# Kernel tuning notes

Measured on AMD Instinct MI355X. Metric: run time of the kernel, lower is better.

The kernel has to match this reference:

```python
import jax, jax.numpy as jnp
import numpy as np

V, E, H, B, T = 50257, 1024, 1024, 64, 512  # vocab, embed, hidden, batch, steps
PADDING_TOKEN = 0


def setup_inputs() -> dict:
    key = jax.random.key(0)
    ks = jax.random.split(key, 6)
    s = 0.02
    emb = jax.random.normal(ks[0], (V, E), jnp.float32) * s
    emb = emb.at[PADDING_TOKEN].set(0.0)  # padding_idx row is zero
    W_ih = jax.random.normal(ks[1], (4 * H, E), jnp.float32) * s   # torch LSTMCell weight_ih
    W_hh = jax.random.normal(ks[2], (4 * H, H), jnp.float32) * s   # torch LSTMCell weight_hh
    W_cls = jax.random.normal(ks[3], (V, H), jnp.float32) * s      # classifier weight [out,in]
    b_cls = jnp.zeros((V,), jnp.float32)                            # classifier bias
    batch_reviews = jax.random.randint(ks[4], (B, T), 0, V)
    return dict(batch_reviews=batch_reviews, emb=emb, W_ih=W_ih, W_hh=W_hh,
                W_cls=W_cls, b_cls=b_cls)


def _lstm_scan(x_tbe, W_ih, W_hh):
    # torch.nn.LSTMCell math (bias=False); gate order: i, f, g, o
    Bn = x_tbe.shape[1]
    Hn = W_hh.shape[1]

    def cell(carry, x_be):
        h, c = carry
        gates = x_be @ W_ih.T + h @ W_hh.T              # [B, 4H]
        i, f, g, o = jnp.split(gates, 4, axis=-1)
        c2 = jax.nn.sigmoid(f) * c + jax.nn.sigmoid(i) * jnp.tanh(g)
        h2 = jax.nn.sigmoid(o) * jnp.tanh(c2)
        return (h2, c2), None

    init = (jnp.zeros((Bn, Hn), x_tbe.dtype), jnp.zeros((Bn, Hn), x_tbe.dtype))
    (h, c), _ = jax.lax.scan(cell, init, x_tbe)
    return h, c


def reference(batch_reviews, emb, W_ih, W_hh, W_cls, b_cls):
    x = emb[batch_reviews]               # [B, T, E] embedding lookup
    x_tbe = jnp.transpose(x, (1, 0, 2))  # [T, B, E] for time-major scan
    h, c = _lstm_scan(x_tbe, W_ih, W_hh) # final (h, c) state only
    logits = h @ W_cls.T + b_cls         # [B, V]
    return logits, h, c
```

## Files before the change

### kernel.cpp

```cpp
#include <hip/hip_runtime.h>

#define Bn 64
#define Tn 512
#define En 1024
#define Hn 1024
#define Vn 50257
#define CHUNK 64
#define NCHUNK (Tn / CHUNK)
#define AGENT __HIP_MEMORY_SCOPE_AGENT

typedef __attribute__((ext_vector_type(8))) short short8;
typedef __attribute__((ext_vector_type(4))) float f32x4;
typedef __attribute__((ext_vector_type(4))) unsigned int u32x4;

__device__ __forceinline__ unsigned short f2bf(float f) {
    union { float f; unsigned u; } x; x.f = f;
    unsigned r = x.u + 0x7FFFu + ((x.u >> 16) & 1u);
    return (unsigned short)(r >> 16);
}
__device__ __forceinline__ float bf2f(unsigned short u) {
    union { unsigned u; float f; } x; x.u = ((unsigned)u) << 16; return x.f;
}
__device__ __forceinline__ float sigm(float x) { return 1.0f / (1.0f + __expf(-x)); }
__device__ __forceinline__ float tanh_fast(float x) {
    float e = __expf(2.0f * x);
    return (e - 1.0f) / (e + 1.0f);
}

#define LDH(dst, base, IMM)                                                  \
    asm volatile("global_load_dwordx4 %0, %1, off offset:" #IMM " sc0 sc1"   \
                 : "=v"(dst) : "v"(base) : "memory")
#define VMW(N) do { asm volatile("s_waitcnt vmcnt(" #N ")" ::: "memory");    \
                    __builtin_amdgcn_sched_barrier(0); } while (0)
#define ISSUE_GRP(buf, O0, O1, O2, O3)                                       \
    do {                                                                     \
        LDH((buf)[0], ap0, O0); LDH((buf)[1], ap0, O1);                      \
        LDH((buf)[2], ap0, O2); LDH((buf)[3], ap0, O3);                      \
        LDH((buf)[4], ap1, O0); LDH((buf)[5], ap1, O1);                      \
        LDH((buf)[6], ap1, O2); LDH((buf)[7], ap1, O3);                      \
    } while (0)
#define MFMA_GRP(buf, jb)                                                    \
    do {                                                                     \
        _Pragma("unroll")                                                    \
        for (int jj = 0; jj < 4; ++jj) {                                     \
            union { u32x4 u; short8 s; } f0, f1;                             \
            f0.u = (buf)[jj]; f1.u = (buf)[4 + jj];                          \
            acc[0][0] = __builtin_amdgcn_mfma_f32_16x16x32_bf16(f0.s, breg[0][(jb) + jj], acc[0][0], 0, 0, 0); \
            acc[0][1] = __builtin_amdgcn_mfma_f32_16x16x32_bf16(f0.s, breg[1][(jb) + jj], acc[0][1], 0, 0, 0); \
            acc[1][0] = __builtin_amdgcn_mfma_f32_16x16x32_bf16(f1.s, breg[0][(jb) + jj], acc[1][0], 0, 0, 0); \
            acc[1][1] = __builtin_amdgcn_mfma_f32_16x16x32_bf16(f1.s, breg[1][(jb) + jj], acc[1][1], 0, 0, 0); \
        }                                                                    \
    } while (0)

__global__ __launch_bounds__(256)
void cvt_f32_bf16(const float* __restrict__ src, unsigned short* __restrict__ dst, int n4) {
    int i = blockIdx.x * 256 + threadIdx.x;
    if (i < n4) {
        float4 v = reinterpret_cast<const float4*>(src)[i];
        ushort4 o;
        o.x = f2bf(v.x); o.y = f2bf(v.y); o.z = f2bf(v.z); o.w = f2bf(v.w);
        reinterpret_cast<ushort4*>(dst)[i] = o;
    }
}

__global__ __launch_bounds__(256)
void gather_x(const int* __restrict__ tokens, const float* __restrict__ emb,
              unsigned short* __restrict__ X, int t0) {
    const int r = blockIdx.x;
    const int trel = r >> 6, b = r & 63;
    const int tok = tokens[b * Tn + t0 + trel];
    const float* src = emb + (size_t)tok * En;
    const int k = threadIdx.x * 4;
    float4 v = *reinterpret_cast<const float4*>(src + k);
    ushort4 o;
    o.x = f2bf(v.x); o.y = f2bf(v.y); o.z = f2bf(v.z); o.w = f2bf(v.w);
    *reinterpret_cast<ushort4*>(X + (size_t)r * En + k) = o;
}

__device__ __forceinline__ void gemm_tile(
    const unsigned short* __restrict__ X, const unsigned short* __restrict__ Wih,
    unsigned short* __restrict__ G, int bx, int by,
    unsigned short (*As)[72], unsigned short (*Bs)[72], int tid)
{
    const int w = tid >> 6, l = tid & 63;
    const int wr = w >> 1, wc = w & 1;
    const int koff = (l >> 4) * 8;

    f32x4 acc[4][4];
#pragma unroll
    for (int i = 0; i < 4; ++i)
#pragma unroll
        for (int j = 0; j < 4; ++j) acc[i][j] = (f32x4){0.f, 0.f, 0.f, 0.f};

    for (int kk = 0; kk < En / 64; ++kk) {
        __syncthreads();
#pragma unroll
        for (int j = 0; j < 4; ++j) {
            const int u = tid * 4 + j;
            const int row = u >> 3, ku = (u & 7) * 8;
            *reinterpret_cast<short8*>(&As[row][ku]) =
                *reinterpret_cast<const short8*>(X + (size_t)(by * 128 + row) * En + kk * 64 + ku);
            *reinterpret_cast<short8*>(&Bs[row][ku]) =
                *reinterpret_cast<const short8*>(Wih + (size_t)(bx * 128 + row) * En + kk * 64 + ku);
        }
        __syncthreads();

#pragma unroll
        for (int kc = 0; kc < 2; ++kc) {
            const int k0 = kc * 32 + koff;
            short8 af[4], bf[4];
#pragma unroll
            for (int i = 0; i < 4; ++i)
                af[i] = *reinterpret_cast<const short8*>(&As[wr * 64 + i * 16 + (l & 15)][k0]);
#pragma unroll
            for (int j = 0; j < 4; ++j)
                bf[j] = *reinterpret_cast<const short8*>(&Bs[wc * 64 + j * 16 + (l & 15)][k0]);
#pragma unroll
            for (int i = 0; i < 4; ++i)
#pragma unroll
                for (int j = 0; j < 4; ++j)
                    acc[i][j] = __builtin_amdgcn_mfma_f32_16x16x32_bf16(af[i], bf[j], acc[i][j], 0, 0, 0);
        }
    }

    const int rr = 4 * (l >> 4);
#pragma unroll
    for (int i = 0; i < 4; ++i) {
        const int row = by * 128 + wr * 64 + i * 16 + rr;
#pragma unroll
        for (int j = 0; j < 4; ++j) {
            const int col = bx * 128 + wc * 64 + j * 16 + (l & 15);
#pragma unroll
            for (int r = 0; r < 4; ++r)
                G[(size_t)(row + r) * 4096 + col] = f2bf(acc[i][j][r]);
        }
    }
}

__global__ __launch_bounds__(256)
void gemm_gin(const unsigned short* __restrict__ X, const unsigned short* __restrict__ Wih,
              unsigned short* __restrict__ G) {
    __shared__ __align__(16) unsigned short As[128][72];
    __shared__ __align__(16) unsigned short Bs[128][72];
    gemm_tile(X, Wih, G, blockIdx.x & 31, blockIdx.x >> 5, As, Bs, threadIdx.x);
}

__global__ __launch_bounds__(256, 1)
void lstm_fused(const unsigned short* __restrict__ Gcur, unsigned short* __restrict__ Gnext,
                const unsigned short* __restrict__ Xnext, const unsigned short* __restrict__ Wih,
                const unsigned short* __restrict__ Whh,
                unsigned short* __restrict__ h0, unsigned short* __restrict__ h1,
                float* __restrict__ c_state, unsigned* __restrict__ flags, int t0, int do_gemm,
                float* __restrict__ out_h, float* __restrict__ out_c)
{
    __shared__ __align__(16) char smem[2 * 128 * 72 * 2];

    const int tid = threadIdx.x;

    if (blockIdx.x >= 128) {
        if (!do_gemm) return;
        unsigned short (*As)[72] = reinterpret_cast<unsigned short(*)[72]>(smem);
        unsigned short (*Bs)[72] = reinterpret_cast<unsigned short(*)[72]>(smem + 128 * 72 * 2);
        const int base = (blockIdx.x - 128) * 8;
        for (int tt = 0; tt < 8; ++tt) {
            const int tile = base + tt;
            gemm_tile(Xnext, Wih, Gnext, tile & 31, tile >> 5, As, Bs, tid);
        }
        return;
    }

    typedef float RedT[2][2][64][4];
    RedT* red = reinterpret_cast<RedT*>(smem);

    const int b = blockIdx.x;
    const int w = tid >> 6, l = tid & 63;
    const int kh = w & 1, rh = w >> 1;
    const int koff = (l >> 4) * 8;
    const int lc = l & 15;
    const int hcol = b * 8 + (l & 7);

    short8 breg[2][16];
#pragma unroll
    for (int ct = 0; ct < 2; ++ct) {
        const int gate = ct * 2 + (lc >> 3);
        const unsigned short* wrow = Whh + ((size_t)gate * Hn + (b * 8 + (lc & 7))) * Hn;
#pragma unroll
        for (int j = 0; j < 16; ++j)
            breg[ct][j] = *reinterpret_cast<const short8*>(wrow + (kh * 16 + j) * 32 + koff);
    }

    float c_reg[2][4];
    if (kh == 0) {
#pragma unroll
        for (int rt = 0; rt < 2; ++rt)
#pragma unroll
            for (int r = 0; r < 4; ++r)
                c_reg[rt][r] = c_state[(rh * 32 + rt * 16 + ((l >> 4) << 2) + r) * Hn + hcol];
    }

    const int sg = lc >> 3;
    const int gc0 = sg * Hn + hcol;
    const int gc1 = (2 + sg) * Hn + hcol;

    unsigned short gp0[2][4], gp1[2][4];
    if (kh == 0) {
#pragma unroll
        for (int rt = 0; rt < 2; ++rt) {
            const int rowbase = rh * 32 + rt * 16 + ((l >> 4) << 2);
#pragma unroll
            for (int r = 0; r < 4; ++r) {
                gp0[rt][r] = Gcur[(size_t)(rowbase + r) * 4096 + gc0];
                gp1[rt][r] = Gcur[(size_t)(rowbase + r) * 4096 + gc1];
            }
        }
    }

    const unsigned* myflag = &flags[(kh * 64 + l) * 32];

    for (int s = 0; s < CHUNK; ++s) {
        const int t = t0 + s;
        const unsigned short* hin = (t & 1) ? h1 : h0;
        unsigned short* hout = (t & 1) ? h0 : h1;

        {
            const unsigned target = (unsigned)t;
            int guard = 0;
            while (__hip_atomic_load(myflag, __ATOMIC_RELAXED, AGENT) < target &&
                   guard < (1 << 16)) {
                __builtin_amdgcn_s_sleep(1);
                ++guard;
            }
        }
        __builtin_amdgcn_sched_barrier(0);

        const unsigned short* ap0 =
            hin + (size_t)(rh * 32 + (l & 15)) * Hn + kh * 512 + koff;
        const unsigned short* ap1 =
            hin + (size_t)(rh * 32 + 16 + (l & 15)) * Hn + kh * 512 + koff;

        f32x4 acc[2][2];
        acc[0][0] = acc[0][1] = acc[1][0] = acc[1][1] = (f32x4){0.f, 0.f, 0.f, 0.f};

        u32x4 bufA[8], bufB[8], bufC[8], bufD[8];
        ISSUE_GRP(bufA, 0,   64,  128, 192);
        ISSUE_GRP(bufB, 256, 320, 384, 448);
        ISSUE_GRP(bufC, 512, 576, 640, 704);
        ISSUE_GRP(bufD, 768, 832, 896, 960);

        VMW(24); MFMA_GRP(bufA, 0);
        VMW(16); MFMA_GRP(bufB, 4);
        VMW(8);  MFMA_GRP(bufC, 8);
        VMW(0);  MFMA_GRP(bufD, 12);

        if (kh == 1) {
#pragma unroll
            for (int rt = 0; rt < 2; ++rt)
#pragma unroll
                for (int ct = 0; ct < 2; ++ct)
                    *reinterpret_cast<f32x4*>(&red[rh][rt][ct][l][0]) = acc[rt][ct];
        }
        __syncthreads();

        if (kh == 0) {
#pragma unroll
            for (int rt = 0; rt < 2; ++rt) {
                const int rowbase = rh * 32 + rt * 16 + ((l >> 4) << 2);
                f32x4 a0 = acc[rt][0] + *reinterpret_cast<f32x4*>(&red[rh][rt][0][l][0]);
                f32x4 a1 = acc[rt][1] + *reinterpret_cast<f32x4*>(&red[rh][rt][1][l][0]);
#pragma unroll
                for (int r = 0; r < 4; ++r) {
                    float v0 = a0[r] + bf2f(gp0[rt][r]);
                    float v1 = a1[r] + bf2f(gp1[rt][r]);
                    float p0 = __shfl_xor(v0, 8);
                    float p1 = __shfl_xor(v1, 8);
                    float iv = (l & 8) ? p0 : v0;
                    float fv = (l & 8) ? v0 : p0;
                    float gv = (l & 8) ? p1 : v1;
                    float ov = (l & 8) ? v1 : p1;
                    float cn = sigm(fv) * c_reg[rt][r] + sigm(iv) * tanh_fast(gv);
                    float hn = sigm(ov) * tanh_fast(cn);
                    c_reg[rt][r] = cn;
                    unsigned hb = f2bf(hn);
                    unsigned partner = (unsigned)__shfl_xor((int)hb, 1);
                    if (!(l & 8) && !(l & 1)) {
                        unsigned val = (hb & 0xFFFFu) | (partner << 16);
                        __hip_atomic_store(
                            (unsigned*)(hout + (size_t)(rowbase + r) * Hn + hcol),
                            val, __ATOMIC_RELAXED, AGENT);
                    }
                    if (t == Tn - 1 && !(l & 8)) {
                        out_h[(rowbase + r) * Hn + hcol] = hn;
                        out_c[(rowbase + r) * Hn + hcol] = cn;
                    }
                }
            }
        }

        asm volatile("s_waitcnt vmcnt(0)" ::: "memory");
        __syncthreads();
        if (tid == 0)
            __hip_atomic_store(&flags[b * 32], (unsigned)(t + 1), __ATOMIC_RELAXED, AGENT);

        if (kh == 0 && s + 1 < CHUNK) {
            const unsigned short* Gt = Gcur + (size_t)(s + 1) * Bn * 4096;
#pragma unroll
            for (int rt = 0; rt < 2; ++rt) {
                const int rowbase = rh * 32 + rt * 16 + ((l >> 4) << 2);
#pragma unroll
                for (int r = 0; r < 4; ++r) {
                    gp0[rt][r] = Gt[(size_t)(rowbase + r) * 4096 + gc0];
                    gp1[rt][r] = Gt[(size_t)(rowbase + r) * 4096 + gc1];
                }
            }
        }
    }

    if (kh == 0 && !(l & 8)) {
#pragma unroll
        for (int rt = 0; rt < 2; ++rt)
#pragma unroll
            for (int r = 0; r < 4; ++r)
                c_state[(rh * 32 + rt * 16 + ((l >> 4) << 2) + r) * Hn + hcol] = c_reg[rt][r];
    }
}

__global__ __launch_bounds__(256)
void classifier(const unsigned short* __restrict__ h,
                const float* __restrict__ Wcls, const float* __restrict__ bcls,
                float* __restrict__ logits)
{
    __shared__ __align__(16) unsigned short Al[64][72];
    __shared__ __align__(16) unsigned short Bl[64][72];

    const int tid = threadIdx.x;
    const int v0 = blockIdx.x * 64;
    const int w = tid >> 6, l = tid & 63;
    const int lrow = tid >> 2, q = tid & 3;
    const int v = v0 + lrow;

    const unsigned short* hrow = h + lrow * Hn;
    const float* wrow = Wcls + (size_t)v * Hn;

    f32x4 acc[4];
#pragma unroll
    for (int ct = 0; ct < 4; ++ct) acc[ct] = (f32x4){0.f, 0.f, 0.f, 0.f};

    const int arow = w * 16 + (l & 15);
    const int koff = (l >> 4) * 8;

    for (int ch = 0; ch < 16; ++ch) {
        const int k0 = ch * 64;
        __syncthreads();
#pragma unroll
        for (int i2 = 0; i2 < 4; ++i2) {
            const int k = q * 4 + i2 * 16;
            *reinterpret_cast<ushort4*>(&Al[lrow][k]) =
                *reinterpret_cast<const ushort4*>(hrow + k0 + k);
            if (v < Vn) {
                float4 x = *reinterpret_cast<const float4*>(wrow + k0 + k);
                Bl[lrow][k + 0] = f2bf(x.x); Bl[lrow][k + 1] = f2bf(x.y);
                Bl[lrow][k + 2] = f2bf(x.z); Bl[lrow][k + 3] = f2bf(x.w);
            } else {
                ushort4 z; z.x = z.y = z.z = z.w = 0;
                *reinterpret_cast<ushort4*>(&Bl[lrow][k]) = z;
            }
        }
        __syncthreads();

        short8 a0 = *reinterpret_cast<const short8*>(&Al[arow][koff]);
        short8 a1 = *reinterpret_cast<const short8*>(&Al[arow][32 + koff]);
#pragma unroll
        for (int ct = 0; ct < 4; ++ct) {
            const int bcol = ct * 16 + (l & 15);
            short8 b0 = *reinterpret_cast<const short8*>(&Bl[bcol][koff]);
            short8 b1 = *reinterpret_cast<const short8*>(&Bl[bcol][32 + koff]);
            acc[ct] = __builtin_amdgcn_mfma_f32_16x16x32_bf16(a0, b0, acc[ct], 0, 0, 0);
            acc[ct] = __builtin_amdgcn_mfma_f32_16x16x32_bf16(a1, b1, acc[ct], 0, 0, 0);
        }
    }

    const int rr0 = w * 16 + (l >> 4) * 4;
#pragma unroll
    for (int ct = 0; ct < 4; ++ct) {
        const int vv = v0 + ct * 16 + (l & 15);
        if (vv < Vn) {
            float bb = bcls[vv];
#pragma unroll
            for (int r = 0; r < 4; ++r)
                logits[(size_t)(rr0 + r) * Vn + vv] = acc[ct][r] + bb;
        }
    }
}

extern "C" void kernel_launch(void* const* d_in, const int* in_sizes, int n_in,
                              void* d_out, int out_size, void* d_ws, size_t ws_size,
                              hipStream_t stream)
{
    const int*   tokens = (const int*)d_in[0];
    const float* emb    = (const float*)d_in[1];
    const float* W_ih   = (const float*)d_in[2];
    const float* W_hh   = (const float*)d_in[3];
    const float* W_cls  = (const float*)d_in[4];
    const float* b_cls  = (const float*)d_in[5];
    float* out = (float*)d_out;

    char* ws = (char*)d_ws;
    unsigned short* hbuf0 = (unsigned short*)ws;
    unsigned short* hbuf1 = (unsigned short*)(ws + 131072);
    float*          cst   = (float*)(ws + 262144);
    unsigned*       flags = (unsigned*)(ws + 524288);
    unsigned short* Wih_b = (unsigned short*)(ws + 540672);
    unsigned short* Whh_b = (unsigned short*)(ws + 540672 + 8388608);
    unsigned short* Xb    = (unsigned short*)(ws + 540672 + 2 * 8388608);
    unsigned short* Gb0   = (unsigned short*)(ws + 540672 + 3 * 8388608);
    unsigned short* Gb1   = (unsigned short*)(ws + 540672 + 3 * 8388608 + 33554432);

    hipMemsetAsync(ws, 0, 540672, stream);

    const int n4 = (4 * Hn * En) / 4;
    cvt_f32_bf16<<<n4 / 256, 256, 0, stream>>>(W_ih, Wih_b, n4);
    cvt_f32_bf16<<<n4 / 256, 256, 0, stream>>>(W_hh, Whh_b, n4);

    float* out_h = out + (size_t)Bn * Vn;
    float* out_c = out_h + Bn * Hn;

    gather_x<<<CHUNK * Bn, 256, 0, stream>>>(tokens, emb, Xb, 0);
    gemm_gin<<<32 * 32, 256, 0, stream>>>(Xb, Wih_b, Gb0);

    unsigned short* Gbuf[2] = {Gb0, Gb1};
    for (int c = 0; c < NCHUNK; ++c) {
        const int do_gemm = (c + 1 < NCHUNK) ? 1 : 0;
        if (do_gemm)
            gather_x<<<CHUNK * Bn, 256, 0, stream>>>(tokens, emb, Xb, (c + 1) * CHUNK);
        lstm_fused<<<256, 256, 0, stream>>>(Gbuf[c & 1], Gbuf[(c + 1) & 1], Xb,
                                            Wih_b, Whh_b, hbuf0, hbuf1,
                                            cst, flags, c * CHUNK, do_gemm,
                                            out_h, out_c);
    }

    classifier<<<(Vn + 63) / 64, 256, 0, stream>>>(hbuf0, W_cls, b_cls, out);
}
```

Measured before the change: 4.258 ms.

## Split recurrent matvec into front/back K-halves with partial-sum handoff and step-major gate layout

The 128 recurrent blocks are reorganised: each of 64 front blocks owns 16 hidden columns (all four gates) and the first K half, while 64 back blocks compute the second K half and publish fp32 partials through global memory under a separate flag. Only front blocks do the cell update and signal the h-ready flags, so each step waits on 64 flags instead of 128, polled with a wave-wide any. The input-gate GEMM now writes a time/column-major layout, so per-step gate preloads become vector loads. The extra partial-sum handoff adds a global round trip and a second dependency chain to every timestep.

```diff
diff --git a/kernel.cpp b/kernel.cpp
--- a/kernel.cpp
+++ b/kernel.cpp
@@ -30,6 +30,9 @@
 #define LDH(dst, base, IMM)                                                  \
     asm volatile("global_load_dwordx4 %0, %1, off offset:" #IMM " sc0 sc1"   \
                  : "=v"(dst) : "v"(base) : "memory")
+#define STHI(addr, data, IMM)                                                \
+    asm volatile("global_store_dwordx4 %0, %1, off offset:" #IMM " sc0 sc1"  \
+                 :: "v"(addr), "v"(data) : "memory")
 #define VMW(N) do { asm volatile("s_waitcnt vmcnt(" #N ")" ::: "memory");    \
                     __builtin_amdgcn_sched_barrier(0); } while (0)
 #define ISSUE_GRP(buf, O0, O1, O2, O3)                                       \
@@ -39,16 +42,17 @@
         LDH((buf)[4], ap1, O0); LDH((buf)[5], ap1, O1);                      \
         LDH((buf)[6], ap1, O2); LDH((buf)[7], ap1, O3);                      \
     } while (0)
-#define MFMA_GRP(buf, jb)                                                    \
+#define MFMA_G4(buf, jb)                                                     \
     do {                                                                     \
         _Pragma("unroll")                                                    \
         for (int jj = 0; jj < 4; ++jj) {                                     \
             union { u32x4 u; short8 s; } f0, f1;                             \
             f0.u = (buf)[jj]; f1.u = (buf)[4 + jj];                          \
-            acc[0][0] = __builtin_amdgcn_mfma_f32_16x16x32_bf16(f0.s, breg[0][(jb) + jj], acc[0][0], 0, 0, 0); \
-            acc[0][1] = __builtin_amdgcn_mfma_f32_16x16x32_bf16(f0.s, breg[1][(jb) + jj], acc[0][1], 0, 0, 0); \
-            acc[1][0] = __builtin_amdgcn_mfma_f32_16x16x32_bf16(f1.s, breg[0][(jb) + jj], acc[1][0], 0, 0, 0); \
-            acc[1][1] = __builtin_amdgcn_mfma_f32_16x16x32_bf16(f1.s, breg[1][(jb) + jj], acc[1][1], 0, 0, 0); \
+            _Pragma("unroll")                                                \
+            for (int ct = 0; ct < 4; ++ct) {                                 \
+                acc[0][ct] = __builtin_amdgcn_mfma_f32_16x16x32_bf16(f0.s, breg[ct][(jb) + jj], acc[0][ct], 0, 0, 0); \
+                acc[1][ct] = __builtin_amdgcn_mfma_f32_16x16x32_bf16(f1.s, breg[ct][(jb) + jj], acc[1][ct], 0, 0, 0); \
+            }                                                                \
         }                                                                    \
     } while (0)
 
@@ -79,7 +83,7 @@
 
 __device__ __forceinline__ void gemm_tile(
     const unsigned short* __restrict__ X, const unsigned short* __restrict__ Wih,
-    unsigned short* __restrict__ G, int bx, int by,
+    unsigned short* __restrict__ G2, int bx, int by,
     unsigned short (*As)[72], unsigned short (*Bs)[72], int tid)
 {
     const int w = tid >> 6, l = tid & 63;
@@ -126,23 +130,25 @@
     const int rr = 4 * (l >> 4);
 #pragma unroll
     for (int i = 0; i < 4; ++i) {
-        const int row = by * 128 + wr * 64 + i * 16 + rr;
+        const int grow = by * 128 + wr * 64 + i * 16 + rr;
+        const int sI = grow >> 6, br = grow & 63;
 #pragma unroll
         for (int j = 0; j < 4; ++j) {
             const int col = bx * 128 + wc * 64 + j * 16 + (l & 15);
-#pragma unroll
-            for (int r = 0; r < 4; ++r)
-                G[(size_t)(row + r) * 4096 + col] = f2bf(acc[i][j][r]);
+            ushort4 o;
+            o.x = f2bf(acc[i][j][0]); o.y = f2bf(acc[i][j][1]);
+            o.z = f2bf(acc[i][j][2]); o.w = f2bf(acc[i][j][3]);
+            *reinterpret_cast<ushort4*>(G2 + (size_t)sI * 262144 + (size_t)col * 64 + br) = o;
         }
     }
 }
 
 __global__ __launch_bounds__(256)
 void gemm_gin(const unsigned short* __restrict__ X, const unsigned short* __restrict__ Wih,
-              unsigned short* __restrict__ G) {
+              unsigned short* __restrict__ G2) {
     __shared__ __align__(16) unsigned short As[128][72];
     __shared__ __align__(16) unsigned short Bs[128][72];
-    gemm_tile(X, Wih, G, blockIdx.x & 31, blockIdx.x >> 5, As, Bs, threadIdx.x);
+    gemm_tile(X, Wih, G2, blockIdx.x & 31, blockIdx.x >> 5, As, Bs, threadIdx.x);
 }
 
 __global__ __launch_bounds__(256, 1)
@@ -150,7 +156,9 @@
                 const unsigned short* __restrict__ Xnext, const unsigned short* __restrict__ Wih,
                 const unsigned short* __restrict__ Whh,
                 unsigned short* __restrict__ h0, unsigned short* __restrict__ h1,
-                float* __restrict__ c_state, unsigned* __restrict__ flags, int t0, int do_gemm,
+                float* __restrict__ c_state, unsigned* __restrict__ flags,
+                unsigned* __restrict__ pflags, float* __restrict__ partials,
+                int t0, int do_gemm,
                 float* __restrict__ out_h, float* __restrict__ out_c)
 {
     __shared__ __align__(16) char smem[2 * 128 * 72 * 2];
@@ -169,53 +177,46 @@
         return;
     }
 
-    typedef float RedT[2][2][64][4];
+    typedef float RedT[2][4][64][4];
     RedT* red = reinterpret_cast<RedT*>(smem);
 
     const int b = blockIdx.x;
+    const int front = (b < 64) ? 1 : 0;
+    const int pb = front ? b : (b - 64);
     const int w = tid >> 6, l = tid & 63;
-    const int kh = w & 1, rh = w >> 1;
+    const int kh2 = w & 1, rh = w >> 1;
+    const int lc = l & 15;
     const int koff = (l >> 4) * 8;
-    const int lc = l & 15;
-    const int hcol = b * 8 + (l & 7);
-
-    short8 breg[2][16];
-#pragma unroll
-    for (int ct = 0; ct < 2; ++ct) {
-        const int gate = ct * 2 + (lc >> 3);
-        const unsigned short* wrow = Whh + ((size_t)gate * Hn + (b * 8 + (lc & 7))) * Hn;
-#pragma unroll
-        for (int j = 0; j < 16; ++j)
-            breg[ct][j] = *reinterpret_cast<const short8*>(wrow + (kh * 16 + j) * 32 + koff);
+    const int kbase = (front ? 0 : 512) + kh2 * 256;
+
+    short8 breg[4][8];
+#pragma unroll
+    for (int ct = 0; ct < 4; ++ct) {
+        const unsigned short* wrow =
+            Whh + (size_t)(ct * Hn + pb * 16 + lc) * Hn + kbase + koff;
+#pragma unroll
+        for (int j = 0; j < 8; ++j)
+            breg[ct][j] = *reinterpret_cast<const short8*>(wrow + j * 32);
     }
 
     float c_reg[2][4];
-    if (kh == 0) {
+    if (front && kh2 == 0) {
 #pragma unroll
         for (int rt = 0; rt < 2; ++rt)
 #pragma unroll
             for (int r = 0; r < 4; ++r)
-                c_reg[rt][r] = c_state[(rh * 32 + rt * 16 + ((l >> 4) << 2) + r) * Hn + hcol];
-    }
-
-    const int sg = lc >> 3;
-    const int gc0 = sg * Hn + hcol;
-    const int gc1 = (2 + sg) * Hn + hcol;
-
-    unsigned short gp0[2][4], gp1[2][4];
-    if (kh == 0) {
-#pragma unroll
-        for (int rt = 0; rt < 2; ++rt) {
-            const int rowbase = rh * 32 + rt * 16 + ((l >> 4) << 2);
-#pragma unroll
-            for (int r = 0; r < 4; ++r) {
-                gp0[rt][r] = Gcur[(size_t)(rowbase + r) * 4096 + gc0];
-                gp1[rt][r] = Gcur[(size_t)(rowbase + r) * 4096 + gc1];
-            }
-        }
-    }
-
-    const unsigned* myflag = &flags[(kh * 64 + l) * 32];
+                c_reg[rt][r] = c_state[(rh * 32 + rt * 16 + (l >> 4) * 4 + r) * Hn + pb * 16 + lc];
+    }
+
+    ushort4 gp[2][4];
+    if (front && kh2 == 0) {
+#pragma unroll
+        for (int rt = 0; rt < 2; ++rt)
+#pragma unroll
+            for (int ct = 0; ct < 4; ++ct)
+                gp[rt][ct] = *reinterpret_cast<const ushort4*>(
+                    Gcur + (size_t)(ct * 1024 + pb * 16 + lc) * 64 + rh * 32 + rt * 16 + (l >> 4) * 4);
+    }
 
     for (int s = 0; s < CHUNK; ++s) {
         const int t = t0 + s;
@@ -223,104 +224,143 @@
         unsigned short* hout = (t & 1) ? h0 : h1;
 
         {
-            const unsigned target = (unsigned)t;
-            int guard = 0;
-            while (__hip_atomic_load(myflag, __ATOMIC_RELAXED, AGENT) < target &&
-                   guard < (1 << 16)) {
+            unsigned fv = __hip_atomic_load(&flags[l * 32], __ATOMIC_RELAXED, AGENT);
+            int g = 0;
+            while (__any(fv < (unsigned)t) && g < (1 << 16)) {
                 __builtin_amdgcn_s_sleep(1);
-                ++guard;
+                fv = __hip_atomic_load(&flags[l * 32], __ATOMIC_RELAXED, AGENT);
+                ++g;
             }
         }
         __builtin_amdgcn_sched_barrier(0);
 
-        const unsigned short* ap0 =
-            hin + (size_t)(rh * 32 + (l & 15)) * Hn + kh * 512 + koff;
-        const unsigned short* ap1 =
-            hin + (size_t)(rh * 32 + 16 + (l & 15)) * Hn + kh * 512 + koff;
-
-        f32x4 acc[2][2];
-        acc[0][0] = acc[0][1] = acc[1][0] = acc[1][1] = (f32x4){0.f, 0.f, 0.f, 0.f};
-
-        u32x4 bufA[8], bufB[8], bufC[8], bufD[8];
+        const unsigned short* ap0 = hin + (size_t)(rh * 32 + lc) * Hn + kbase + koff;
+        const unsigned short* ap1 = hin + (size_t)(rh * 32 + 16 + lc) * Hn + kbase + koff;
+
+        f32x4 acc[2][4];
+#pragma unroll
+        for (int rt = 0; rt < 2; ++rt)
+#pragma unroll
+            for (int ct = 0; ct < 4; ++ct) acc[rt][ct] = (f32x4){0.f, 0.f, 0.f, 0.f};
+
+        u32x4 bufA[8], bufB[8];
         ISSUE_GRP(bufA, 0,   64,  128, 192);
         ISSUE_GRP(bufB, 256, 320, 384, 448);
-        ISSUE_GRP(bufC, 512, 576, 640, 704);
-        ISSUE_GRP(bufD, 768, 832, 896, 960);
-
-        VMW(24); MFMA_GRP(bufA, 0);
-        VMW(16); MFMA_GRP(bufB, 4);
-        VMW(8);  MFMA_GRP(bufC, 8);
-        VMW(0);  MFMA_GRP(bufD, 12);
-
-        if (kh == 1) {
+
+        VMW(8); MFMA_G4(bufA, 0);
+        VMW(0); MFMA_G4(bufB, 4);
+
+        if (kh2 == 1) {
 #pragma unroll
             for (int rt = 0; rt < 2; ++rt)
 #pragma unroll
-                for (int ct = 0; ct < 2; ++ct)
+                for (int ct = 0; ct < 4; ++ct)
                     *reinterpret_cast<f32x4*>(&red[rh][rt][ct][l][0]) = acc[rt][ct];
         }
         __syncthreads();
 
-        if (kh == 0) {
-#pragma unroll
-            for (int rt = 0; rt < 2; ++rt) {
-                const int rowbase = rh * 32 + rt * 16 + ((l >> 4) << 2);
-                f32x4 a0 = acc[rt][0] + *reinterpret_cast<f32x4*>(&red[rh][rt][0][l][0]);
-                f32x4 a1 = acc[rt][1] + *reinterpret_cast<f32x4*>(&red[rh][rt][1][l][0]);
-#pragma unroll
-                for (int r = 0; r < 4; ++r) {
-                    float v0 = a0[r] + bf2f(gp0[rt][r]);
-                    float v1 = a1[r] + bf2f(gp1[rt][r]);
-                    float p0 = __shfl_xor(v0, 8);
-                    float p1 = __shfl_xor(v1, 8);
-                    float iv = (l & 8) ? p0 : v0;
-                    float fv = (l & 8) ? v0 : p0;
-                    float gv = (l & 8) ? p1 : v1;
-                    float ov = (l & 8) ? v1 : p1;
-                    float cn = sigm(fv) * c_reg[rt][r] + sigm(iv) * tanh_fast(gv);
-                    float hn = sigm(ov) * tanh_fast(cn);
-                    c_reg[rt][r] = cn;
-                    unsigned hb = f2bf(hn);
-                    unsigned partner = (unsigned)__shfl_xor((int)hb, 1);
-                    if (!(l & 8) && !(l & 1)) {
-                        unsigned val = (hb & 0xFFFFu) | (partner << 16);
-                        __hip_atomic_store(
-                            (unsigned*)(hout + (size_t)(rowbase + r) * Hn + hcol),
-                            val, __ATOMIC_RELAXED, AGENT);
-                    }
-                    if (t == Tn - 1 && !(l & 8)) {
-                        out_h[(rowbase + r) * Hn + hcol] = hn;
-                        out_c[(rowbase + r) * Hn + hcol] = cn;
+        if (kh2 == 0) {
+#pragma unroll
+            for (int rt = 0; rt < 2; ++rt)
+#pragma unroll
+                for (int ct = 0; ct < 4; ++ct)
+                    acc[rt][ct] = acc[rt][ct] + *reinterpret_cast<f32x4*>(&red[rh][rt][ct][l][0]);
+
+            float* Pp = partials + (size_t)(pb * 2 + (t & 1)) * 4096 + (rh * 64 + l) * 32;
+
+            if (front) {
+                {
+                    unsigned pv = __hip_atomic_load(&pflags[pb * 32], __ATOMIC_RELAXED, AGENT);
+                    int g = 0;
+                    while (__any(pv < (unsigned)(t + 1)) && g < (1 << 16)) {
+                        __builtin_amdgcn_s_sleep(1);
+                        pv = __hip_atomic_load(&pflags[pb * 32], __ATOMIC_RELAXED, AGENT);
+                        ++g;
                     }
                 }
+                __builtin_amdgcn_sched_barrier(0);
+                u32x4 pp[8];
+                LDH(pp[0], Pp, 0);  LDH(pp[1], Pp, 16); LDH(pp[2], Pp, 32);  LDH(pp[3], Pp, 48);
+                LDH(pp[4], Pp, 64); LDH(pp[5], Pp, 80); LDH(pp[6], Pp, 96);  LDH(pp[7], Pp, 112);
+                VMW(0);
+#pragma unroll
+                for (int rt = 0; rt < 2; ++rt)
+#pragma unroll
+                    for (int ct = 0; ct < 4; ++ct) {
+                        union { u32x4 u; f32x4 f; } cv; cv.u = pp[rt * 4 + ct];
+                        acc[rt][ct] = acc[rt][ct] + cv.f;
+                    }
+
+#pragma unroll
+                for (int rt = 0; rt < 2; ++rt) {
+                    const unsigned short* gi = reinterpret_cast<const unsigned short*>(&gp[rt][0]);
+                    const unsigned short* gf = reinterpret_cast<const unsigned short*>(&gp[rt][1]);
+                    const unsigned short* gg = reinterpret_cast<const unsigned short*>(&gp[rt][2]);
+                    const unsigned short* go = reinterpret_cast<const unsigned short*>(&gp[rt][3]);
+#pragma unroll
+                    for (int r = 0; r < 4; ++r) {
+                        float iv = acc[rt][0][r] + bf2f(gi[r]);
+                        float fv = acc[rt][1][r] + bf2f(gf[r]);
+                        float gv = acc[rt][2][r] + bf2f(gg[r]);
+                        float ov = acc[rt][3][r] + bf2f(go[r]);
+                        float cn = sigm(fv) * c_reg[rt][r] + sigm(iv) * tanh_fast(gv);
+                        float hn = sigm(ov) * tanh_fast(cn);
+                        c_reg[rt][r] = cn;
+                        const int row = rh * 32 + rt * 16 + (l >> 4) * 4 + r;
+                        unsigned hb = f2bf(hn);
+                        unsigned partner = (unsigned)__shfl_xor((int)hb, 1);
+                        if (!(l & 1)) {
+                            unsigned val = (hb & 0xFFFFu) | (partner << 16);
+                            __hip_atomic_store(
+                                (unsigned*)(hout + (size_t)row * Hn + pb * 16 + lc),
+                                val, __ATOMIC_RELAXED, AGENT);
+                        }
+                        if (t == Tn - 1) {
+                            out_h[row * Hn + pb * 16 + lc] = hn;
+                            out_c[row * Hn + pb * 16 + lc] = cn;
+                        }
+                    }
+                }
+                asm volatile("s_waitcnt vmcnt(0)" ::: "memory");
+            } else {
+                union { f32x4 f; u32x4 u; } d;
+                d.f = acc[0][0]; STHI(Pp, d.u, 0);
+                d.f = acc[0][1]; STHI(Pp, d.u, 16);
+                d.f = acc[0][2]; STHI(Pp, d.u, 32);
+                d.f = acc[0][3]; STHI(Pp, d.u, 48);
+                d.f = acc[1][0]; STHI(Pp, d.u, 64);
+                d.f = acc[1][1]; STHI(Pp, d.u, 80);
+                d.f = acc[1][2]; STHI(Pp, d.u, 96);
+                d.f = acc[1][3]; STHI(Pp, d.u, 112);
+                asm volatile("s_waitcnt vmcnt(0)" ::: "memory");
             }
         }
-
-        asm volatile("s_waitcnt vmcnt(0)" ::: "memory");
-        __syncthreads();
-        if (tid == 0)
-            __hip_atomic_store(&flags[b * 32], (unsigned)(t + 1), __ATOMIC_RELAXED, AGENT);
-
-        if (kh == 0 && s + 1 < CHUNK) {
-            const unsigned short* Gt = Gcur + (size_t)(s + 1) * Bn * 4096;
-#pragma unroll
-            for (int rt = 0; rt < 2; ++rt) {
-                const int rowbase = rh * 32 + rt * 16 + ((l >> 4) << 2);
-#pragma unroll
-                for (int r = 0; r < 4; ++r) {
-                    gp0[rt][r] = Gt[(size_t)(rowbase + r) * 4096 + gc0];
-                    gp1[rt][r] = Gt[(size_t)(rowbase + r) * 4096 + gc1];
-                }
-            }
-        }
-    }
-
-    if (kh == 0 && !(l & 8)) {
+        __syncthreads();
+
+        if (tid == 0) {
+            if (front)
+                __hip_atomic_store(&flags[b * 32], (unsigned)(t + 1), __ATOMIC_RELAXED, AGENT);
+            else
+                __hip_atomic_store(&pflags[pb * 32], (unsigned)(t + 1), __ATOMIC_RELAXED, AGENT);
+        }
+
+        if (front && kh2 == 0 && s + 1 < CHUNK) {
+            const unsigned short* Gt = Gcur + (size_t)(s + 1) * 262144;
+#pragma unroll
+            for (int rt = 0; rt < 2; ++rt)
+#pragma unroll
+                for (int ct = 0; ct < 4; ++ct)
+                    gp[rt][ct] = *reinterpret_cast<const ushort4*>(
+                        Gt + (size_t)(ct * 1024 + pb * 16 + lc) * 64 + rh * 32 + rt * 16 + (l >> 4) * 4);
+        }
+    }
+
+    if (front && kh2 == 0) {
 #pragma unroll
         for (int rt = 0; rt < 2; ++rt)
 #pragma unroll
             for (int r = 0; r < 4; ++r)
-                c_state[(rh * 32 + rt * 16 + ((l >> 4) << 2) + r) * Hn + hcol] = c_reg[rt][r];
+                c_state[(rh * 32 + rt * 16 + (l >> 4) * 4 + r) * Hn + pb * 16 + lc] = c_reg[rt][r];
     }
 }
 
@@ -405,17 +445,19 @@
     float* out = (float*)d_out;
 
     char* ws = (char*)d_ws;
-    unsigned short* hbuf0 = (unsigned short*)ws;
-    unsigned short* hbuf1 = (unsigned short*)(ws + 131072);
-    float*          cst   = (float*)(ws + 262144);
-    unsigned*       flags = (unsigned*)(ws + 524288);
-    unsigned short* Wih_b = (unsigned short*)(ws + 540672);
-    unsigned short* Whh_b = (unsigned short*)(ws + 540672 + 8388608);
-    unsigned short* Xb    = (unsigned short*)(ws + 540672 + 2 * 8388608);
-    unsigned short* Gb0   = (unsigned short*)(ws + 540672 + 3 * 8388608);
-    unsigned short* Gb1   = (unsigned short*)(ws + 540672 + 3 * 8388608 + 33554432);
-
-    hipMemsetAsync(ws, 0, 540672, stream);
+    unsigned short* hbuf0  = (unsigned short*)ws;
+    unsigned short* hbuf1  = (unsigned short*)(ws + 131072);
+    float*          cst    = (float*)(ws + 262144);
+    unsigned*       flags  = (unsigned*)(ws + 524288);
+    unsigned*       pflags = (unsigned*)(ws + 540672);
+    float*          parts  = (float*)(ws + 557056);
+    unsigned short* Wih_b  = (unsigned short*)(ws + 2654208);
+    unsigned short* Whh_b  = (unsigned short*)(ws + 2654208 + 8388608);
+    unsigned short* Xb     = (unsigned short*)(ws + 2654208 + 2 * 8388608);
+    unsigned short* Gb0    = (unsigned short*)(ws + 2654208 + 3 * 8388608);
+    unsigned short* Gb1    = (unsigned short*)(ws + 2654208 + 3 * 8388608 + 33554432);
+
+    hipMemsetAsync(ws, 0, 557056, stream);
 
     const int n4 = (4 * Hn * En) / 4;
     cvt_f32_bf16<<<n4 / 256, 256, 0, stream>>>(W_ih, Wih_b, n4);
@@ -434,8 +476,8 @@
             gather_x<<<CHUNK * Bn, 256, 0, stream>>>(tokens, emb, Xb, (c + 1) * CHUNK);
         lstm_fused<<<256, 256, 0, stream>>>(Gbuf[c & 1], Gbuf[(c + 1) & 1], Xb,
                                             Wih_b, Whh_b, hbuf0, hbuf1,
-                                            cst, flags, c * CHUNK, do_gemm,
-                                            out_h, out_c);
+                                            cst, flags, pflags, parts,
+                                            c * CHUNK, do_gemm, out_h, out_c);
     }
 
     classifier<<<(Vn + 63) / 64, 256, 0, stream>>>(hbuf0, W_cls, b_cls, out);
```

New measurement: 5.034 ms. +18.2%, slower.
